# Optimization experiments

Hardware: AMD Instinct MI355X
Metric: run time of the kernel (lower is better)

## Reference

```python
import jax, jax.numpy as jnp
import numpy as np

WIN, DIL, PAD, H = 5, 1, 2, 8  # window, dilation, unfold padding, num_heads
C = 256
EPS = 1e-5

def _ln(z, g, b):
    m = jnp.mean(z, axis=-1, keepdims=True)
    v = jnp.mean((z - m) ** 2, axis=-1, keepdims=True)
    return (z - m) * jax.lax.rsqrt(v + EPS) * g + b

def setup_inputs() -> dict:
    key = jax.random.key(0)
    ks = jax.random.split(key, 16)
    s = 0.02
    d = {
        'x': jax.random.normal(ks[0], (32, C, 64, 25), jnp.float32),
        'ln1_g': jnp.ones((C,), jnp.float32), 'ln1_b': jnp.zeros((C,), jnp.float32),
        'q_w': jax.random.normal(ks[1], (C, C)) * s, 'q_b': jnp.zeros((C,)),
        'qa_w': jax.random.normal(ks[2], (C, H)) * s, 'qa_b': jnp.zeros((H,)),
        'k_w': jax.random.normal(ks[3], (C, C)) * s, 'k_b': jnp.zeros((C,)),
        'ka_w': jax.random.normal(ks[4], (C, H)) * s, 'ka_b': jnp.zeros((H,)),
        'v_w': jax.random.normal(ks[5], (C, C)) * s, 'v_b': jnp.zeros((C,)),
        't_w': jax.random.normal(ks[6], (C, C)) * s, 't_b': jnp.zeros((C,)),
        'p_w': jax.random.normal(ks[7], (C, C)) * s, 'p_b': jnp.zeros((C,)),
        'ffn_g': jnp.ones((C,)), 'ffn_b': jnp.zeros((C,)),
        'w1': jax.random.normal(ks[8], (C, C)) * s, 'b1': jnp.zeros((C,)),
        'w2': jax.random.normal(ks[9], (C, C)) * s, 'b2': jnp.zeros((C,)),
    }
    return d

def reference(x, ln1_g, ln1_b, q_w, q_b, qa_w, qa_b, k_w, k_b, ka_w, ka_b,
              v_w, v_b, t_w, t_b, p_w, p_b, ffn_g, ffn_b, w1, b1, w2, b2):
    N, Cc, T, V = x.shape
    hc = Cc // H
    scale = 1.0 / np.sqrt(hc)
    B, L = N * T, WIN * V
    xp = jnp.pad(x, ((0, 0), (0, 0), (PAD, PAD), (0, 0)))
    win = jnp.stack([xp[:, :, k * DIL:k * DIL + T, :] for k in range(WIN)], axis=2)  # (N,C,W,T,V)
    wx = win.transpose(0, 3, 2, 4, 1).reshape(B, L, Cc)
    nx = _ln(wx, ln1_g, ln1_b)
    # attention: softmax-pooled query
    q = nx @ q_w + q_b                                      # (B,L,C)
    qw = jax.nn.softmax(((q @ qa_w + qa_b) * scale).transpose(0, 2, 1), axis=-1)  # (B,H,L)
    qh = q.reshape(B, L, H, hc).transpose(0, 2, 1, 3)       # (B,H,L,hc)
    pq = jnp.einsum('bhl,bhld->bhd', qw, qh)                # (B,H,hc)
    k_ = nx @ k_w + k_b
    kq = k_ * pq.reshape(B, 1, Cc)
    kw = jax.nn.softmax(((kq @ ka_w + ka_b) * scale).transpose(0, 2, 1), axis=-1)
    kh = k_.reshape(B, L, H, hc).transpose(0, 2, 1, 3)
    pk = jnp.einsum('bhl,bhld->bhd', kw, kh)                # (B,H,hc)
    v_ = nx @ v_w + v_b
    vh = v_.reshape(B, L, H, hc).transpose(0, 2, 1, 3)
    kv = (vh * pk[:, :, None, :]).transpose(0, 2, 1, 3).reshape(B, L, Cc)
    kvh = (kv @ t_w + t_b).reshape(B, L, H, hc).transpose(0, 2, 1, 3)
    att = ((kvh + qh).transpose(0, 2, 1, 3).reshape(B, L, Cc)) @ p_w + p_b
    # average over window, residual with flattened x
    att = att.reshape(B, WIN, V, Cc).mean(axis=1)           # (B,V,C)
    att = att + x.transpose(0, 2, 3, 1).reshape(B, V, Cc)
    # FFN residual block
    f = _ln(att, ffn_g, ffn_b)
    f = jax.nn.gelu(f @ w1 + b1, approximate=False) @ w2 + b2
    y = f + att
    return y.reshape(N, T, V, Cc).transpose(0, 3, 1, 2)     # (N,C,T,V)
```

## Files before the change

### kernel.cpp

```cpp
#include <hip/hip_runtime.h>
#include <hip/hip_bf16.h>

typedef unsigned short u16b;
typedef __attribute__((ext_vector_type(8))) short short8;
typedef __attribute__((ext_vector_type(4))) float floatx4;

#define DEV static __device__ __forceinline__

DEV float sh2f(unsigned short s) { union { unsigned u; float f; } c; c.u = ((unsigned)s) << 16; return c.f; }
DEV unsigned short f2b(float f) {
    unsigned u = __float_as_uint(f);
    u += 0x7FFF + ((u >> 16) & 1);
    return (unsigned short)(u >> 16);
}

DEV void gload_lds16(const u16b* g, u16b* l) {
    __builtin_amdgcn_global_load_lds((const __attribute__((address_space(1))) void*)g,
                                     (__attribute__((address_space(3))) void*)l, 16, 0, 0);
}

constexpr int O_LN1G = 0, O_LN1B = 256, O_QB = 512, O_KB = 768, O_VB = 1024,
              O_TB = 1280, O_PB = 1536, O_FFNG = 1792, O_FFNB = 2048,
              O_B1 = 2304, O_B2 = 2560, O_QAB = 2816, O_KAB = 2824,
              O_QAW = 2832, O_KAW = 4880, O_CV = 6928;

__global__ void detect_k(const unsigned* __restrict__ xw, int* __restrict__ flag) {
    __shared__ int cnt;
    if (threadIdx.x == 0) cnt = 0;
    __syncthreads();
    int my = 0;
    for (int i = threadIdx.x; i < 4096; i += 256) {
        unsigned w = xw[i];
        unsigned e0 = (w >> 7) & 0xFFu;
        if (e0 >= 0xC0u) my++;
    }
    atomicAdd(&cnt, my);
    __syncthreads();
    if (threadIdx.x == 0) flag[0] = (cnt > 64) ? 1 : 0;
}

DEV unsigned short load_cvt(const void* src, size_t idx, int fp32) {
    return fp32 ? f2b(((const float*)src)[idx]) : ((const u16b*)src)[idx];
}

struct VecTab { const void* p[15]; int off[15]; int n[15]; };

__global__ __launch_bounds__(256)
void convert_vecs_k(VecTab tab, const int* __restrict__ flag, u16b* __restrict__ sv) {
    int e = blockIdx.x, fp32 = flag[0];
    const void* s = tab.p[e];
    int n = tab.n[e], off = tab.off[e];
    for (int i = threadIdx.x; i < n; i += 256)
        sv[off + i] = load_cvt(s, i, fp32);
}

struct W8 { const void* p[8]; unsigned dstoff[8]; unsigned rstride[8]; };

__global__ void wtrans_k(W8 tab, u16b* __restrict__ base, const int* __restrict__ flag) {
    __shared__ u16b tile[32][33];
    int fp32 = flag[0];
    const void* src = tab.p[blockIdx.z];
    u16b* dst = base + tab.dstoff[blockIdx.z];
    unsigned rs = tab.rstride[blockIdx.z];
    int c0 = blockIdx.x * 32, r0 = blockIdx.y * 32;
    int tx = threadIdx.x, ty = threadIdx.y;
#pragma unroll
    for (int i = 0; i < 32; i += 8)
        tile[ty + i][tx] = load_cvt(src, (size_t)(r0 + ty + i) * 256 + c0 + tx, fp32);
    __syncthreads();
#pragma unroll
    for (int i = 0; i < 32; i += 8)
        dst[(size_t)(c0 + ty + i) * rs + r0 + tx] = tile[tx][ty + i];
}

__global__ __launch_bounds__(256)
void transpose_in_k(const void* __restrict__ src, u16b* __restrict__ dst,
                    int rows, int cols, const int* __restrict__ flag) {
    __shared__ u16b tile[32][36];
    int fp32 = flag[0];
    int c0 = blockIdx.x * 32, r0 = blockIdx.y * 32;
    size_t zb = (size_t)blockIdx.z * rows * cols;
    int tid = threadIdx.x;
    int r = tid >> 3, c4 = (tid & 7) * 4;
    size_t sidx = zb + (size_t)(r0 + r) * cols + c0 + c4;
    if (fp32) {
        const float4 f4 = *(const float4*)((const float*)src + sidx);
        tile[r][c4]     = f2b(f4.x);
        tile[r][c4 + 1] = f2b(f4.y);
        tile[r][c4 + 2] = f2b(f4.z);
        tile[r][c4 + 3] = f2b(f4.w);
    } else {
        *(ushort4*)&tile[r][c4] = *(const ushort4*)((const u16b*)src + sidx);
    }
    __syncthreads();
    int c = tid >> 3, r4 = (tid & 7) * 4;
    ushort4 o;
    o.x = tile[r4][c]; o.y = tile[r4 + 1][c]; o.z = tile[r4 + 2][c]; o.w = tile[r4 + 3][c];
    *(ushort4*)&dst[zb + (size_t)(c0 + c) * rows + r0 + r4] = o;
}

__global__ __launch_bounds__(256)
void rowstats_k(const u16b* __restrict__ src, float2* __restrict__ st,
                int valid, int total) {
    int wv = threadIdx.x >> 6, lane = threadIdx.x & 63;
    int r = blockIdx.x * 4 + wv;
    if (r >= total) return;
    if (r >= valid) { if (lane == 0) st[r] = make_float2(0.f, 0.f); return; }
    int c = lane * 4;
    ushort4 raw = *(const ushort4*)&src[(size_t)r * 256 + c];
    float x0 = sh2f(raw.x), x1 = sh2f(raw.y), x2 = sh2f(raw.z), x3 = sh2f(raw.w);
    float s  = x0 + x1 + x2 + x3;
    float sq = x0 * x0 + x1 * x1 + x2 * x2 + x3 * x3;
#pragma unroll
    for (int o = 32; o; o >>= 1) { s += __shfl_xor(s, o); sq += __shfl_xor(sq, o); }
    float mean = s * (1.f / 256.f);
    float var  = sq * (1.f / 256.f) - mean * mean;
    if (lane == 0) st[r] = make_float2(mean, rsqrtf(var + 1e-5f));
}

__global__ __launch_bounds__(256)
void cvec_k(const u16b* __restrict__ pT, u16b* __restrict__ sv) {
    int j = threadIdx.x;
    float acc = sh2f(sv[O_PB + j]);
    const u16b* row = pT + (size_t)j * 256;
    for (int i = 0; i < 256; i += 8) {
        short8 t8 = *(const short8*)&sv[O_TB + i];
        short8 p8 = *(const short8*)&row[i];
#pragma unroll
        for (int u = 0; u < 8; ++u)
            acc += sh2f((unsigned short)t8[u]) * sh2f((unsigned short)p8[u]);
    }
    sv[O_CV + j] = f2b(acc);
}

template <int EPI, int LNA, int XY = 0, int STATS = 0>
__global__ __launch_bounds__(256, 4)
void gemm256(const u16b* __restrict__ A, int aStride, int K,
             const u16b* __restrict__ Wt,
             const u16b* __restrict__ bias, const u16b* __restrict__ addm,
             u16b* __restrict__ out, size_t osParam,
             const float2* __restrict__ stats, const float2* __restrict__ stats2,
             const u16b* __restrict__ gvec, const u16b* __restrict__ bvec,
             float2* __restrict__ statOut, const int* __restrict__ flag) {
    constexpr bool ALDS = (LNA == 0);
    __shared__ u16b As[64 * 72];
    __shared__ u16b Bs[8448];
    __shared__ float sg[256], sb[256];
    const int tid = threadIdx.x;
    const int m0 = (XY ? blockIdx.y : blockIdx.x) * 64;
    const int n0 = (XY ? blockIdx.x : blockIdx.y) * 128;
    const int wv = tid >> 6, lane = tid & 63;
    const int wrow = (wv >> 1) * 32, wcol = (wv & 1) * 64;
    const int fr = lane & 15;
    const int fq = lane >> 4;
    floatx4 acc[2][4];
    const floatx4 zero = {0.f, 0.f, 0.f, 0.f};
#pragma unroll
    for (int i = 0; i < 2; ++i)
#pragma unroll
        for (int j = 0; j < 4; ++j) acc[i][j] = zero;

    float2 strow[2];
    if (LNA) {
        sg[tid] = sh2f(gvec[tid]);
        sb[tid] = sh2f(bvec[tid]);
#pragma unroll
        for (int kk = 0; kk < 2; ++kk) {
            int r = m0 + (tid >> 3) + kk * 32;
            if (LNA == 2) {
                float2 a = stats[r], b = stats2[r];
                float mean = (a.x + b.x) * (1.f / 256.f);
                float var  = (a.y + b.y) * (1.f / 256.f) - mean * mean;
                strow[kk] = make_float2(mean, rsqrtf(var + 1e-5f));
            } else {
                strow[kk] = stats[r];
            }
        }
        __syncthreads();
    }

    for (int kt = 0; kt < K; kt += 64) {
        if (ALDS) {
#pragma unroll
            for (int kk = 0; kk < 2; ++kk) {
                int chunk = tid + kk * 256;
                int row = chunk >> 3, col = (chunk & 7) * 8;
                int scol = col ^ ((row & 7) << 3);
                gload_lds16(&A[(size_t)(m0 + row) * aStride + kt + scol], &As[chunk * 8]);
            }
        } else {
#pragma unroll
            for (int kk = 0; kk < 2; ++kk) {
                int chunk = tid + kk * 256;
                int row = chunk >> 3, col = (chunk & 7) * 8;
                union { uint4 u; unsigned short h[8]; } rw;
                rw.u = *(const uint4*)&A[(size_t)(m0 + row) * aStride + kt + col];
#pragma unroll
                for (int j = 0; j < 8; ++j) {
                    float f = sh2f(rw.h[j]);
                    f = (f - strow[kk].x) * strow[kk].y * sg[kt + col + j] + sb[kt + col + j];
                    rw.h[j] = f2b(f);
                }
                *(uint4*)&As[row * 72 + col] = rw.u;
            }
        }
#pragma unroll
        for (int kk = 0; kk < 4; ++kk) {
            int chunk = tid + kk * 256;
            int row = chunk >> 3, col = (chunk & 7) * 8;
            int scol = col ^ ((row & 7) << 3);
            gload_lds16(&Wt[(size_t)(n0 + row) * K + kt + scol], &Bs[chunk * 8]);
        }
        __syncthreads();
#pragma unroll
        for (int s = 0; s < 2; ++s) {
            short8 af[2], bfr[4];
#pragma unroll
            for (int i = 0; i < 2; ++i) {
                int ar = wrow + i * 16 + fr;
                if (ALDS)
                    af[i] = *(const short8*)((const char*)As +
                              ((ar * 128 + s * 64 + fq * 16) ^ ((ar & 7) << 4)));
                else
                    af[i] = *(short8*)&As[ar * 72 + s * 32 + fq * 8];
            }
#pragma unroll
            for (int j = 0; j < 4; ++j) {
                int br = wcol + j * 16 + fr;
                bfr[j] = *(const short8*)((const char*)Bs +
                          ((br * 128 + s * 64 + fq * 16) ^ ((br & 7) << 4)));
            }
#pragma unroll
            for (int i = 0; i < 2; ++i)
#pragma unroll
                for (int j = 0; j < 4; ++j)
                    acc[i][j] = __builtin_amdgcn_mfma_f32_16x16x32_bf16(af[i], bfr[j], acc[i][j], 0, 0, 0);
        }
        __syncthreads();
    }
    float bv[4];
#pragma unroll
    for (int j = 0; j < 4; ++j) bv[j] = bias ? sh2f(bias[n0 + wcol + j * 16 + fr]) : 0.f;

    if (EPI == 5) {
        u16b* CT = Bs;
#pragma unroll
        for (int kk = 0; kk < 4; ++kk) {
            int chunk = tid + kk * 256;
            int row = chunk >> 4, c8 = (chunk & 15) * 8;
            *(uint4*)&CT[row * 132 + c8] = *(const uint4*)&addm[(size_t)(m0 + row) * 256 + n0 + c8];
        }
        __syncthreads();
        int fp32o = flag[0];
#pragma unroll
        for (int i = 0; i < 2; ++i) {
            int lr0 = wrow + i * 16 + fq * 4;
            int row0 = m0 + lr0;
            int n = row0 / 1600;
            int tv = row0 - n * 1600;
#pragma unroll
            for (int j = 0; j < 4; ++j) {
                int lc = wcol + j * 16 + fr;
                int col = n0 + lc;
                float v4[4];
#pragma unroll
                for (int r = 0; r < 4; ++r)
                    v4[r] = acc[i][j][r] + bv[j] + sh2f(CT[(lr0 + r) * 132 + lc]);
                size_t oidx = ((size_t)n * 256 + col) * 1600 + tv;
                if (fp32o) {
                    float4 o = {v4[0], v4[1], v4[2], v4[3]};
                    *(float4*)((float*)out + oidx) = o;
                } else {
                    ushort4 o;
                    o.x = f2b(v4[0]); o.y = f2b(v4[1]); o.z = f2b(v4[2]); o.w = f2b(v4[3]);
                    *(ushort4*)&out[oidx] = o;
                }
            }
        }
    } else if (EPI == 2) {
        float* CTf = (float*)Bs;
#pragma unroll
        for (int half = 0; half < 2; ++half) {
            if ((wrow >> 5) == half) {
#pragma unroll
                for (int i = 0; i < 2; ++i)
#pragma unroll
                    for (int r = 0; r < 4; ++r) {
                        int lrow = i * 16 + fq * 4 + r;
#pragma unroll
                        for (int j = 0; j < 4; ++j)
                            CTf[lrow * 132 + wcol + j * 16 + fr] = acc[i][j][r] + bv[j];
                    }
            }
            __syncthreads();
#pragma unroll
            for (int kk = 0; kk < 2; ++kk) {
                int chunk = tid + kk * 256;
                int row = chunk >> 4, c8 = (chunk & 15) * 8;
                int grow = m0 + half * 32 + row, gcol = n0 + c8;
                union { uint4 u; unsigned short h[8]; } am, ow;
                am.u = *(const uint4*)&addm[(size_t)grow * 256 + gcol];
                float s1 = 0.f, s2 = 0.f;
#pragma unroll
                for (int u8 = 0; u8 < 8; ++u8) {
                    float v = CTf[row * 132 + c8 + u8] + sh2f(am.h[u8]);
                    s1 += v; s2 += v * v;
                    ow.h[u8] = f2b(v);
                }
                if (STATS) {
#pragma unroll
                    for (int mm = 1; mm < 16; mm <<= 1) {
                        s1 += __shfl_xor(s1, mm);
                        s2 += __shfl_xor(s2, mm);
                    }
                    if ((tid & 15) == 0)
                        statOut[(size_t)(n0 >> 7) * 51200 + grow] = make_float2(s1, s2);
                }
                *(uint4*)&out[(size_t)grow * 256 + gcol] = ow.u;
            }
            __syncthreads();
        }
    } else {
        u16b* CT = Bs;
#pragma unroll
        for (int i = 0; i < 2; ++i)
#pragma unroll
            for (int r = 0; r < 4; ++r) {
                int lrow = wrow + i * 16 + fq * 4 + r;
#pragma unroll
                for (int j = 0; j < 4; ++j) {
                    float val = acc[i][j][r] + bv[j];
                    if (EPI == 3) val = 0.5f * val * (1.0f + erff(val * 0.70710678118654752f));
                    CT[lrow * 132 + wcol + j * 16 + fr] = f2b(val);
                }
            }
        __syncthreads();
#pragma unroll
        for (int kk = 0; kk < 4; ++kk) {
            int chunk = tid + kk * 256;
            int row = chunk >> 4, c8 = (chunk & 15) * 8;
            int grow = m0 + row, gcol = n0 + c8;
            uint4 cw = *(const uint4*)&CT[row * 132 + c8];
            if (EPI == 4)      *(uint4*)&out[(size_t)(gcol >> 8) * osParam + (size_t)grow * 256 + (gcol & 255)] = cw;
            else               *(uint4*)&out[(size_t)grow * osParam + gcol] = cw;
        }
    }
}


DEV void logits_union(const u16b* __restrict__ S, const u16b* su, const int* srow,
                      float* slog, const u16b* __restrict__ sv, int aboff, int tid) {
    int wv = tid >> 6, lane = tid & 63;
    int fr = lane & 15, fq = lane >> 4;
    float abv = sh2f(sv[aboff + (fr & 7)]);
    for (int f = wv; f < 10; f += 8) {
        floatx4 acc = {0.f, 0.f, 0.f, 0.f};
        const u16b* Ar = S + (size_t)srow[f * 16 + fr] * 256;
#pragma unroll
        for (int s = 0; s < 8; ++s) {
            short8 a  = *(const short8*)&Ar[s * 32 + fq * 8];
            short8 bb = *(const short8*)&su[fr * 260 + s * 32 + fq * 8];
            acc = __builtin_amdgcn_mfma_f32_16x16x32_bf16(a, bb, acc, 0, 0, 0);
        }
#pragma unroll
        for (int r = 0; r < 4; ++r)
            slog[(f * 16 + fq * 4 + r) * 19 + fr] = (acc[r] + abv) * 0.17677669529663687f;
    }
}

template <int KC>
DEV void softmax16(const float* slog, float* wqA, float* wqB, int tid) {
    int wv = tid >> 6, lane = tid & 63;
#pragma unroll
    for (int c = 0; c < 2; ++c) {
        int combo = wv + c * 8;
        int dt = combo >> 3, h = combo & 7;
        int col = KC ? combo : h;
        const float* src = slog + (size_t)(dt * 25) * 19 + col;
        float v0 = (lane < 125) ? src[lane * 19] : -1e30f;
        float v1 = (lane + 64 < 125) ? src[(lane + 64) * 19] : -1e30f;
        float mx = fmaxf(v0, v1);
#pragma unroll
        for (int o = 32; o; o >>= 1) mx = fmaxf(mx, __shfl_xor(mx, o));
        float e0 = (lane < 125) ? __expf(v0 - mx) : 0.f;
        float e1 = (lane + 64 < 125) ? __expf(v1 - mx) : 0.f;
        float s = e0 + e1;
#pragma unroll
        for (int o = 32; o; o >>= 1) s += __shfl_xor(s, o);
        float inv = 1.f / s;
        float* dst = dt ? wqB : wqA;
        int off = dt ? 25 : 0;
        if (lane < 125) dst[(lane + off) * 9 + h] = e0 * inv;
        if (lane + 64 < 125) dst[(lane + 64 + off) * 9 + h] = e1 * inv;
    }
}

DEV void pool_union(const u16b* __restrict__ S, const int* srow,
                    const float* wqA, const float* wqB, float* scratch,
                    float* out0, float* out1, int tid) {
    int c8 = (tid & 31) * 8, h = c8 >> 5, ls = tid >> 5;
    float a0[8] = {0.f,0.f,0.f,0.f,0.f,0.f,0.f,0.f};
    float a1[8] = {0.f,0.f,0.f,0.f,0.f,0.f,0.f,0.f};
    for (int u = ls; u < 150; u += 16) {
        float w0 = wqA[u * 9 + h];
        float w1 = wqB[u * 9 + h];
        short8 d8 = *(const short8*)&S[(size_t)srow[u] * 256 + c8];
#pragma unroll
        for (int j = 0; j < 8; ++j) {
            float f = sh2f((unsigned short)d8[j]);
            a0[j] += w0 * f;
            a1[j] += w1 * f;
        }
    }
#pragma unroll
    for (int j = 0; j < 8; ++j) {
        a0[j] += __shfl_xor(a0[j], 32);
        a1[j] += __shfl_xor(a1[j], 32);
    }
    int wv = tid >> 6, lane = tid & 63;
    if (lane < 32) {
        float4 lo = {a0[0], a0[1], a0[2], a0[3]}, hi = {a0[4], a0[5], a0[6], a0[7]};
        *(float4*)&scratch[wv * 264 + c8]     = lo;
        *(float4*)&scratch[wv * 264 + c8 + 4] = hi;
    }
    __syncthreads();
    if (tid < 256) {
        float s = 0.f;
#pragma unroll
        for (int q = 0; q < 8; ++q) s += scratch[q * 264 + tid];
        out0[tid] = s;
    }
    __syncthreads();
    if (lane < 32) {
        float4 lo = {a1[0], a1[1], a1[2], a1[3]}, hi = {a1[4], a1[5], a1[6], a1[7]};
        *(float4*)&scratch[wv * 264 + c8]     = lo;
        *(float4*)&scratch[wv * 264 + c8 + 4] = hi;
    }
    __syncthreads();
    if (tid < 256) {
        float s = 0.f;
#pragma unroll
        for (int q = 0; q < 8; ++q) s += scratch[q * 264 + tid];
        out1[tid] = s;
    }
    __syncthreads();
}

DEV void wmean2(const u16b* __restrict__ S, const int* srow,
                const float* scale0, const float* scale1,
                u16b* __restrict__ CB, int base, int nb, int tid) {
    for (int i = tid; i < 800; i += 512) {
        int v = i >> 5, c8 = (i & 31) * 8;
        float s0[8] = {0.f,0.f,0.f,0.f,0.f,0.f,0.f,0.f};
        float s1[8] = {0.f,0.f,0.f,0.f,0.f,0.f,0.f,0.f};
#pragma unroll
        for (int w = 0; w < 6; ++w) {
            short8 d8 = *(const short8*)&S[(size_t)srow[w * 25 + v] * 256 + c8];
#pragma unroll
            for (int j = 0; j < 8; ++j) {
                float f = sh2f((unsigned short)d8[j]);
                if (w < 5)  s0[j] += f;
                if (w >= 1) s1[j] += f;
            }
        }
        unsigned short o0[8], o1[8];
#pragma unroll
        for (int j = 0; j < 8; ++j) {
            float m0 = s0[j] * 0.2f, m1 = s1[j] * 0.2f;
            if (scale0) { m0 *= scale0[c8 + j]; m1 *= scale1[c8 + j]; }
            o0[j] = f2b(m0); o1[j] = f2b(m1);
        }
        *(uint4*)&CB[((size_t)nb * 25 + v) * 512 + base + c8]       = *(uint4*)o0;
        *(uint4*)&CB[((size_t)(nb + 1) * 25 + v) * 512 + base + c8] = *(uint4*)o1;
    }
}

__global__ __launch_bounds__(512)
void pool_fused2(const u16b* __restrict__ qf, const u16b* __restrict__ kf,
                 const u16b* __restrict__ vf, const u16b* __restrict__ sv,
                 u16b* __restrict__ CB) {
    __shared__ int srow[160];
    __shared__ u16b su[16 * 260];
    __shared__ float slog[160 * 19];
    __shared__ float wqA[160 * 9], wqB[160 * 9];
    __shared__ float spq[2][256], spk[2][256];
    int bid = blockIdx.x;
    int b2 = ((bid & 7) << 7) | (bid >> 3);
    int n = b2 >> 5, t0 = (b2 & 31) * 2;
    int nb = n * 64 + t0;
    int tid = threadIdx.x;
    if (tid < 160) {
        int u = tid < 150 ? tid : 149;
        int tl = u / 25, v = u - tl * 25, tt = t0 + tl - 2;
        srow[tid] = ((unsigned)tt < 64u) ? (n * 64 + tt) * 25 + v : 51200;
    }
    for (int i = tid; i < 2048; i += 512) {
        int c = i >> 3, h = i & 7;
        su[h * 260 + c] = sv[O_QAW + i];
    }
    for (int i = tid; i < 1440; i += 512) { wqA[i] = 0.f; wqB[i] = 0.f; }
    __syncthreads();

    logits_union(qf, su, srow, slog, sv, O_QAB, tid);
    __syncthreads();
    softmax16<0>(slog, wqA, wqB, tid);
    __syncthreads();

    pool_union(qf, srow, wqA, wqB, slog, spq[0], spq[1], tid);

    wmean2(qf, srow, nullptr, nullptr, CB, 256, nb, tid);

    for (int i = tid; i < 4096; i += 512) {
        int c = i >> 4, h16 = i & 15;
        float w = sh2f(sv[O_KAW + c * 8 + (h16 & 7)]) * spq[h16 >> 3][c];
        su[h16 * 260 + c] = f2b(w);
    }
    for (int i = tid; i < 1440; i += 512) { wqA[i] = 0.f; wqB[i] = 0.f; }
    __syncthreads();

    logits_union(kf, su, srow, slog, sv, O_KAB, tid);
    __syncthreads();
    softmax16<1>(slog, wqA, wqB, tid);
    __syncthreads();

    pool_union(kf, srow, wqA, wqB, slog, spk[0], spk[1], tid);

    wmean2(vf, srow, spk[0], spk[1], CB, 0, nb, tid);
}

extern "C" void kernel_launch(void* const* d_in, const int* in_sizes, int n_in,
                              void* d_out, int out_size, void* d_ws, size_t ws_size,
                              hipStream_t stream) {
    (void)in_sizes; (void)n_in; (void)out_size; (void)ws_size;
    const void* x    = d_in[0];
    const void* ln1g = d_in[1];  const void* ln1b = d_in[2];
    const void* q_w  = d_in[3];  const void* q_b  = d_in[4];
    const void* qa_w = d_in[5];  const void* qa_b = d_in[6];
    const void* k_w  = d_in[7];  const void* k_b  = d_in[8];
    const void* ka_w = d_in[9];  const void* ka_b = d_in[10];
    const void* v_w  = d_in[11]; const void* v_b  = d_in[12];
    const void* t_w  = d_in[13]; const void* t_b  = d_in[14];
    const void* p_w  = d_in[15]; const void* p_b  = d_in[16];
    const void* ffng = d_in[17]; const void* ffnb = d_in[18];
    const void* w1   = d_in[19]; const void* b1   = d_in[20];
    const void* w2   = d_in[21]; const void* b2   = d_in[22];

    char* ws = (char*)d_ws;
    size_t off = 0;
    auto alloc = [&](size_t bytes) { void* p = ws + off; off += (bytes + 255) & ~(size_t)255; return p; };
    const size_t RPAD = 51328;
    int*    flag = (int*)alloc(256);
    u16b*   sv   = (u16b*)alloc(8192 * 2);
    u16b*   wT   = (u16b*)alloc((size_t)7 * 65536 * 2);
    u16b*   cW   = (u16b*)alloc((size_t)256 * 512 * 2);
    u16b*   xT   = (u16b*)alloc(RPAD * 256 * 2);
    u16b*   Bq   = (u16b*)alloc(RPAD * 256 * 2);
    u16b*   Bk   = (u16b*)alloc(RPAD * 256 * 2);
    u16b*   Bv   = (u16b*)alloc(RPAD * 256 * 2);
    u16b*   CB   = (u16b*)alloc((size_t)51200 * 512 * 2);
    u16b*   att  = (u16b*)alloc((size_t)51200 * 256 * 2);
    float2* st1  = (float2*)alloc(RPAD * 8);
    float2* st2p = (float2*)alloc((size_t)2 * 51200 * 8);

    u16b* pT  = wT + 3 * 65536;
    u16b* tT  = wT + 4 * 65536;
    u16b* w1T = wT + 5 * 65536;
    u16b* w2T = wT + 6 * 65536;

    detect_k<<<1, 256, 0, stream>>>((const unsigned*)x, flag);
    VecTab tab;
    const void* vp[15] = {ln1g, ln1b, q_b, k_b, v_b, t_b, p_b, ffng, ffnb, b1, b2, qa_b, ka_b, qa_w, ka_w};
    const int vo[15] = {O_LN1G, O_LN1B, O_QB, O_KB, O_VB, O_TB, O_PB, O_FFNG, O_FFNB, O_B1, O_B2, O_QAB, O_KAB, O_QAW, O_KAW};
    const int vn[15] = {256, 256, 256, 256, 256, 256, 256, 256, 256, 256, 256, 8, 8, 2048, 2048};
    for (int i = 0; i < 15; ++i) { tab.p[i] = vp[i]; tab.off[i] = vo[i]; tab.n[i] = vn[i]; }
    convert_vecs_k<<<15, 256, 0, stream>>>(tab, flag, sv);

    dim3 tb(32, 8);
    W8 wt;
    const void* wsrc[8] = {q_w, k_w, v_w, p_w, t_w, w1, w2, p_w};
    for (int i = 0; i < 8; ++i) {
        wt.p[i] = wsrc[i];
        wt.dstoff[i] = (i < 7) ? (unsigned)(i * 65536) : (unsigned)((cW + 256) - wT);
        wt.rstride[i] = (i < 7) ? 256u : 512u;
    }
    wtrans_k<<<dim3(8, 8, 8), tb, 0, stream>>>(wt, wT, flag);
    cvec_k<<<1, 256, 0, stream>>>(pT, sv);
    gemm256<0, 0><<<dim3(4, 2), 256, 0, stream>>>(pT, 256, 256, tT, nullptr, nullptr,
                                                  cW, 512, nullptr, nullptr, nullptr, nullptr,
                                                  nullptr, nullptr);
    transpose_in_k<<<dim3(50, 8, 32), 256, 0, stream>>>(x, xT, 256, 1600, flag);
    rowstats_k<<<12832, 256, 0, stream>>>(xT, st1, 51200, 51328);
    gemm256<4, 1, 1><<<dim3(6, 802), 256, 0, stream>>>(xT, 256, 256, wT, sv + O_QB, nullptr,
                                                       Bq, RPAD * 256, st1, nullptr,
                                                       sv + O_LN1G, sv + O_LN1B, nullptr, nullptr);
    pool_fused2<<<1024, 512, 0, stream>>>(Bq, Bk, Bv, sv, CB);
    gemm256<2, 0, 1, 1><<<dim3(2, 800), 256, 0, stream>>>(CB, 512, 512, cW, sv + O_CV, xT,
                                                          att, 256, nullptr, nullptr,
                                                          nullptr, nullptr, st2p, nullptr);
    gemm256<3, 2, 1><<<dim3(2, 800), 256, 0, stream>>>(att, 256, 256, w1T, sv + O_B1, nullptr,
                                                       Bq, 256, st2p, st2p + 51200,
                                                       sv + O_FFNG, sv + O_FFNB, nullptr, nullptr);
    gemm256<5, 0, 1><<<dim3(2, 800), 256, 0, stream>>>(Bq, 256, 256, w2T, sv + O_B2, att,
                                                       (u16b*)d_out, 0, nullptr, nullptr,
                                                       nullptr, nullptr, nullptr, flag);
}
```

Measured before the change: 369.6 us.

## Fuse query-attention logits into QKV GEMM epilogue and merge pool reductions

The QKV projection GEMM now computes the per-row query-attention logits (q @ qa_w) in its epilogue for the q column blocks, writing two partial halves to a new float buffer. The pooling kernel then reads those precomputed logits instead of re-reading q rows and running an MFMA logits pass. The two pooled reductions in pool_union are also split into a sweep and a reduce that share one barrier, which removes several __syncthreads, and one redundant zeroing loop is dropped. The cost is extra epilogue work, a 2048-entry weight load into shared memory, and shuffle reductions inside the GEMM. The logits are also computed from bf16-rounded q values.

```diff
diff --git a/kernel.cpp b/kernel.cpp
--- a/kernel.cpp
+++ b/kernel.cpp
@@ -23,6 +23,7 @@
               O_TB = 1280, O_PB = 1536, O_FFNG = 1792, O_FFNB = 2048,
               O_B1 = 2304, O_B2 = 2560, O_QAB = 2816, O_KAB = 2824,
               O_QAW = 2832, O_KAW = 4880, O_CV = 6928;
+constexpr int RPADC = 51328;
 
 __global__ void detect_k(const unsigned* __restrict__ xw, int* __restrict__ flag) {
     __shared__ int cnt;
@@ -133,7 +134,7 @@
     sv[O_CV + j] = f2b(acc);
 }
 
-template <int EPI, int LNA, int XY = 0, int STATS = 0>
+template <int EPI, int LNA, int XY = 0, int STATS = 0, int LQ = 0>
 __global__ __launch_bounds__(256, 4)
 void gemm256(const u16b* __restrict__ A, int aStride, int K,
              const u16b* __restrict__ Wt,
@@ -141,7 +142,8 @@
              u16b* __restrict__ out, size_t osParam,
              const float2* __restrict__ stats, const float2* __restrict__ stats2,
              const u16b* __restrict__ gvec, const u16b* __restrict__ bvec,
-             float2* __restrict__ statOut, const int* __restrict__ flag) {
+             float2* __restrict__ statOut, const int* __restrict__ flag,
+             const u16b* __restrict__ qawp, float* __restrict__ lqOut) {
     constexpr bool ALDS = (LNA == 0);
     __shared__ u16b As[64 * 72];
     __shared__ u16b Bs[8448];
@@ -322,6 +324,11 @@
         }
     } else {
         u16b* CT = Bs;
+        float* qawf = (float*)As;
+        const bool doLQ = LQ && (n0 < 256);
+        if (doLQ) {
+            for (int i = tid; i < 2048; i += 256) qawf[i] = sh2f(qawp[i]);
+        }
 #pragma unroll
         for (int i = 0; i < 2; ++i)
 #pragma unroll
@@ -343,6 +350,28 @@
             uint4 cw = *(const uint4*)&CT[row * 132 + c8];
             if (EPI == 4)      *(uint4*)&out[(size_t)(gcol >> 8) * osParam + (size_t)grow * 256 + (gcol & 255)] = cw;
             else               *(uint4*)&out[(size_t)grow * osParam + gcol] = cw;
+            if (doLQ) {
+                union { uint4 u; unsigned short h[8]; } cc; cc.u = cw;
+                float s[8] = {0.f, 0.f, 0.f, 0.f, 0.f, 0.f, 0.f, 0.f};
+#pragma unroll
+                for (int j = 0; j < 8; ++j) {
+                    float v = sh2f(cc.h[j]);
+                    const float* qr = qawf + (size_t)(gcol + j) * 8;
+#pragma unroll
+                    for (int h = 0; h < 8; ++h) s[h] += v * qr[h];
+                }
+#pragma unroll
+                for (int mm = 1; mm < 16; mm <<= 1)
+#pragma unroll
+                    for (int h = 0; h < 8; ++h) s[h] += __shfl_xor(s[h], mm);
+                if ((tid & 15) == 0) {
+                    float* dst = lqOut + ((size_t)(n0 >> 7) * RPADC + grow) * 8;
+                    float4 lo = {s[0], s[1], s[2], s[3]};
+                    float4 hi = {s[4], s[5], s[6], s[7]};
+                    *(float4*)dst = lo;
+                    *(float4*)(dst + 4) = hi;
+                }
+            }
         }
     }
 }
@@ -395,9 +424,9 @@
     }
 }
 
-DEV void pool_union(const u16b* __restrict__ S, const int* srow,
-                    const float* wqA, const float* wqB, float* scratch,
-                    float* out0, float* out1, int tid) {
+DEV void pool_sweep2(const u16b* __restrict__ S, const int* srow,
+                     const float* wqA, const float* wqB,
+                     float* scrA, float* scrB, int tid) {
     int c8 = (tid & 31) * 8, h = c8 >> 5, ls = tid >> 5;
     float a0[8] = {0.f,0.f,0.f,0.f,0.f,0.f,0.f,0.f};
     float a1[8] = {0.f,0.f,0.f,0.f,0.f,0.f,0.f,0.f};
@@ -419,31 +448,29 @@
     }
     int wv = tid >> 6, lane = tid & 63;
     if (lane < 32) {
-        float4 lo = {a0[0], a0[1], a0[2], a0[3]}, hi = {a0[4], a0[5], a0[6], a0[7]};
-        *(float4*)&scratch[wv * 264 + c8]     = lo;
-        *(float4*)&scratch[wv * 264 + c8 + 4] = hi;
-    }
-    __syncthreads();
+        float4 lo0 = {a0[0], a0[1], a0[2], a0[3]}, hi0 = {a0[4], a0[5], a0[6], a0[7]};
+        *(float4*)&scrA[wv * 264 + c8]     = lo0;
+        *(float4*)&scrA[wv * 264 + c8 + 4] = hi0;
+        float4 lo1 = {a1[0], a1[1], a1[2], a1[3]}, hi1 = {a1[4], a1[5], a1[6], a1[7]};
+        *(float4*)&scrB[wv * 260 + c8]     = lo1;
+        *(float4*)&scrB[wv * 260 + c8 + 4] = hi1;
+    }
+}
+
+DEV void pool_reduce2(const float* scrA, const float* scrB,
+                      float* out0, float* out1, int tid) {
     if (tid < 256) {
         float s = 0.f;
 #pragma unroll
-        for (int q = 0; q < 8; ++q) s += scratch[q * 264 + tid];
+        for (int q = 0; q < 8; ++q) s += scrA[q * 264 + tid];
         out0[tid] = s;
-    }
-    __syncthreads();
-    if (lane < 32) {
-        float4 lo = {a1[0], a1[1], a1[2], a1[3]}, hi = {a1[4], a1[5], a1[6], a1[7]};
-        *(float4*)&scratch[wv * 264 + c8]     = lo;
-        *(float4*)&scratch[wv * 264 + c8 + 4] = hi;
-    }
-    __syncthreads();
-    if (tid < 256) {
+    } else {
+        int t2 = tid - 256;
         float s = 0.f;
 #pragma unroll
-        for (int q = 0; q < 8; ++q) s += scratch[q * 264 + tid];
-        out1[tid] = s;
-    }
-    __syncthreads();
+        for (int q = 0; q < 8; ++q) s += scrB[q * 260 + t2];
+        out1[t2] = s;
+    }
 }
 
 DEV void wmean2(const u16b* __restrict__ S, const int* srow,
@@ -477,10 +504,10 @@
 
 __global__ __launch_bounds__(512)
 void pool_fused2(const u16b* __restrict__ qf, const u16b* __restrict__ kf,
-                 const u16b* __restrict__ vf, const u16b* __restrict__ sv,
-                 u16b* __restrict__ CB) {
+                 const u16b* __restrict__ vf, const float* __restrict__ Lqp,
+                 const u16b* __restrict__ sv, u16b* __restrict__ CB) {
     __shared__ int srow[160];
-    __shared__ u16b su[16 * 260];
+    __shared__ alignas(16) u16b su[16 * 260];
     __shared__ float slog[160 * 19];
     __shared__ float wqA[160 * 9], wqB[160 * 9];
     __shared__ float spq[2][256], spk[2][256];
@@ -494,28 +521,30 @@
         int tl = u / 25, v = u - tl * 25, tt = t0 + tl - 2;
         srow[tid] = ((unsigned)tt < 64u) ? (n * 64 + tt) * 25 + v : 51200;
     }
-    for (int i = tid; i < 2048; i += 512) {
-        int c = i >> 3, h = i & 7;
-        su[h * 260 + c] = sv[O_QAW + i];
-    }
     for (int i = tid; i < 1440; i += 512) { wqA[i] = 0.f; wqB[i] = 0.f; }
     __syncthreads();
 
-    logits_union(qf, su, srow, slog, sv, O_QAB, tid);
+    for (int i = tid; i < 1200; i += 512) {
+        int u = i >> 3, h = i & 7;
+        size_t row = (size_t)srow[u];
+        float lq = Lqp[row * 8 + h] + Lqp[(size_t)RPADC * 8 + row * 8 + h] + sh2f(sv[O_QAB + h]);
+        slog[u * 19 + h] = lq * 0.17677669529663687f;
+    }
     __syncthreads();
     softmax16<0>(slog, wqA, wqB, tid);
     __syncthreads();
 
-    pool_union(qf, srow, wqA, wqB, slog, spq[0], spq[1], tid);
-
+    pool_sweep2(qf, srow, wqA, wqB, slog, (float*)su, tid);
     wmean2(qf, srow, nullptr, nullptr, CB, 256, nb, tid);
+    __syncthreads();
+    pool_reduce2(slog, (float*)su, spq[0], spq[1], tid);
+    __syncthreads();
 
     for (int i = tid; i < 4096; i += 512) {
         int c = i >> 4, h16 = i & 15;
         float w = sh2f(sv[O_KAW + c * 8 + (h16 & 7)]) * spq[h16 >> 3][c];
         su[h16 * 260 + c] = f2b(w);
     }
-    for (int i = tid; i < 1440; i += 512) { wqA[i] = 0.f; wqB[i] = 0.f; }
     __syncthreads();
 
     logits_union(kf, su, srow, slog, sv, O_KAB, tid);
@@ -523,7 +552,10 @@
     softmax16<1>(slog, wqA, wqB, tid);
     __syncthreads();
 
-    pool_union(kf, srow, wqA, wqB, slog, spk[0], spk[1], tid);
+    pool_sweep2(kf, srow, wqA, wqB, slog, (float*)su, tid);
+    __syncthreads();
+    pool_reduce2(slog, (float*)su, spk[0], spk[1], tid);
+    __syncthreads();
 
     wmean2(vf, srow, spk[0], spk[1], CB, 0, nb, tid);
 }
@@ -548,7 +580,7 @@
     char* ws = (char*)d_ws;
     size_t off = 0;
     auto alloc = [&](size_t bytes) { void* p = ws + off; off += (bytes + 255) & ~(size_t)255; return p; };
-    const size_t RPAD = 51328;
+    const size_t RPAD = RPADC;
     int*    flag = (int*)alloc(256);
     u16b*   sv   = (u16b*)alloc(8192 * 2);
     u16b*   wT   = (u16b*)alloc((size_t)7 * 65536 * 2);
@@ -561,6 +593,7 @@
     u16b*   att  = (u16b*)alloc((size_t)51200 * 256 * 2);
     float2* st1  = (float2*)alloc(RPAD * 8);
     float2* st2p = (float2*)alloc((size_t)2 * 51200 * 8);
+    float*  Lqp  = (float*)alloc((size_t)2 * RPAD * 8 * 4);
 
     u16b* pT  = wT + 3 * 65536;
     u16b* tT  = wT + 4 * 65536;
@@ -587,20 +620,24 @@
     cvec_k<<<1, 256, 0, stream>>>(pT, sv);
     gemm256<0, 0><<<dim3(4, 2), 256, 0, stream>>>(pT, 256, 256, tT, nullptr, nullptr,
                                                   cW, 512, nullptr, nullptr, nullptr, nullptr,
-                                                  nullptr, nullptr);
+                                                  nullptr, nullptr, nullptr, nullptr);
     transpose_in_k<<<dim3(50, 8, 32), 256, 0, stream>>>(x, xT, 256, 1600, flag);
     rowstats_k<<<12832, 256, 0, stream>>>(xT, st1, 51200, 51328);
-    gemm256<4, 1, 1><<<dim3(6, 802), 256, 0, stream>>>(xT, 256, 256, wT, sv + O_QB, nullptr,
-                                                       Bq, RPAD * 256, st1, nullptr,
-                                                       sv + O_LN1G, sv + O_LN1B, nullptr, nullptr);
-    pool_fused2<<<1024, 512, 0, stream>>>(Bq, Bk, Bv, sv, CB);
+    gemm256<4, 1, 1, 0, 1><<<dim3(6, 802), 256, 0, stream>>>(xT, 256, 256, wT, sv + O_QB, nullptr,
+                                                             Bq, RPAD * 256, st1, nullptr,
+                                                             sv + O_LN1G, sv + O_LN1B, nullptr, nullptr,
+                                                             sv + O_QAW, Lqp);
+    pool_fused2<<<1024, 512, 0, stream>>>(Bq, Bk, Bv, Lqp, sv, CB);
     gemm256<2, 0, 1, 1><<<dim3(2, 800), 256, 0, stream>>>(CB, 512, 512, cW, sv + O_CV, xT,
                                                           att, 256, nullptr, nullptr,
-                                                          nullptr, nullptr, st2p, nullptr);
+                                                          nullptr, nullptr, st2p, nullptr,
+                                                          nullptr, nullptr);
     gemm256<3, 2, 1><<<dim3(2, 800), 256, 0, stream>>>(att, 256, 256, w1T, sv + O_B1, nullptr,
                                                        Bq, 256, st2p, st2p + 51200,
-                                                       sv + O_FFNG, sv + O_FFNB, nullptr, nullptr);
+                                                       sv + O_FFNG, sv + O_FFNB, nullptr, nullptr,
+                                                       nullptr, nullptr);
     gemm256<5, 0, 1><<<dim3(2, 800), 256, 0, stream>>>(Bq, 256, 256, w2T, sv + O_B2, att,
                                                        (u16b*)d_out, 0, nullptr, nullptr,
-                                                       nullptr, nullptr, nullptr, flag);
-}
+                                                       nullptr, nullptr, nullptr, flag,
+                                                       nullptr, nullptr);
+}
```

Measured after the change: 426.9 us. +15.5%, slower.

## Fuse LN1 row statistics into QKV GEMM and split pooling reductions

Applied to the files above, without the earlier changes.

Drops the separate rowstats kernel. Each QKV GEMM block now reads its 64 rows of xT in full and computes mean and rstd itself, with an 8-lane shuffle reduction. This removes a kernel launch and a round trip of the stats through global memory, but the stats are recomputed redundantly by each of the 6 column blocks. In the pooling kernel, the two weighted-pool reductions now write to separate scratch buffers so they can be reduced together, which cuts several syncthreads and overlaps the first reduction with wmean2. A redundant zeroing loop is also removed.

```diff
diff --git a/kernel.cpp b/kernel.cpp
--- a/kernel.cpp
+++ b/kernel.cpp
@@ -23,6 +23,7 @@
               O_TB = 1280, O_PB = 1536, O_FFNG = 1792, O_FFNB = 2048,
               O_B1 = 2304, O_B2 = 2560, O_QAB = 2816, O_KAB = 2824,
               O_QAW = 2832, O_KAW = 4880, O_CV = 6928;
+constexpr int VALIDC = 51200;
 
 __global__ void detect_k(const unsigned* __restrict__ xw, int* __restrict__ flag) {
     __shared__ int cnt;
@@ -97,25 +98,6 @@
     ushort4 o;
     o.x = tile[r4][c]; o.y = tile[r4 + 1][c]; o.z = tile[r4 + 2][c]; o.w = tile[r4 + 3][c];
     *(ushort4*)&dst[zb + (size_t)(c0 + c) * rows + r0 + r4] = o;
-}
-
-__global__ __launch_bounds__(256)
-void rowstats_k(const u16b* __restrict__ src, float2* __restrict__ st,
-                int valid, int total) {
-    int wv = threadIdx.x >> 6, lane = threadIdx.x & 63;
-    int r = blockIdx.x * 4 + wv;
-    if (r >= total) return;
-    if (r >= valid) { if (lane == 0) st[r] = make_float2(0.f, 0.f); return; }
-    int c = lane * 4;
-    ushort4 raw = *(const ushort4*)&src[(size_t)r * 256 + c];
-    float x0 = sh2f(raw.x), x1 = sh2f(raw.y), x2 = sh2f(raw.z), x3 = sh2f(raw.w);
-    float s  = x0 + x1 + x2 + x3;
-    float sq = x0 * x0 + x1 * x1 + x2 * x2 + x3 * x3;
-#pragma unroll
-    for (int o = 32; o; o >>= 1) { s += __shfl_xor(s, o); sq += __shfl_xor(sq, o); }
-    float mean = s * (1.f / 256.f);
-    float var  = sq * (1.f / 256.f) - mean * mean;
-    if (lane == 0) st[r] = make_float2(mean, rsqrtf(var + 1e-5f));
 }
 
 __global__ __launch_bounds__(256)
@@ -164,16 +146,40 @@
     if (LNA) {
         sg[tid] = sh2f(gvec[tid]);
         sb[tid] = sh2f(bvec[tid]);
-#pragma unroll
-        for (int kk = 0; kk < 2; ++kk) {
-            int r = m0 + (tid >> 3) + kk * 32;
-            if (LNA == 2) {
+        if (LNA == 1) {
+#pragma unroll
+            for (int kk = 0; kk < 2; ++kk) {
+                int chunk = tid + kk * 256;
+                int row = chunk >> 3, col = (chunk & 7) * 8;
+                float s1 = 0.f, s2 = 0.f;
+#pragma unroll
+                for (int kt2 = 0; kt2 < 256; kt2 += 64) {
+                    union { uint4 u; unsigned short h[8]; } rw;
+                    rw.u = *(const uint4*)&A[(size_t)(m0 + row) * aStride + kt2 + col];
+#pragma unroll
+                    for (int j = 0; j < 8; ++j) {
+                        float f = sh2f(rw.h[j]);
+                        s1 += f; s2 += f * f;
+                    }
+                }
+#pragma unroll
+                for (int mm = 1; mm < 8; mm <<= 1) {
+                    s1 += __shfl_xor(s1, mm);
+                    s2 += __shfl_xor(s2, mm);
+                }
+                float mean = s1 * (1.f / 256.f);
+                float var  = s2 * (1.f / 256.f) - mean * mean;
+                strow[kk] = (m0 + row < VALIDC) ? make_float2(mean, rsqrtf(var + 1e-5f))
+                                                : make_float2(0.f, 0.f);
+            }
+        } else {
+#pragma unroll
+            for (int kk = 0; kk < 2; ++kk) {
+                int r = m0 + (tid >> 3) + kk * 32;
                 float2 a = stats[r], b = stats2[r];
                 float mean = (a.x + b.x) * (1.f / 256.f);
                 float var  = (a.y + b.y) * (1.f / 256.f) - mean * mean;
                 strow[kk] = make_float2(mean, rsqrtf(var + 1e-5f));
-            } else {
-                strow[kk] = stats[r];
             }
         }
         __syncthreads();
@@ -395,9 +401,9 @@
     }
 }
 
-DEV void pool_union(const u16b* __restrict__ S, const int* srow,
-                    const float* wqA, const float* wqB, float* scratch,
-                    float* out0, float* out1, int tid) {
+DEV void pool_sweep2(const u16b* __restrict__ S, const int* srow,
+                     const float* wqA, const float* wqB,
+                     float* scrA, float* scrB, int tid) {
     int c8 = (tid & 31) * 8, h = c8 >> 5, ls = tid >> 5;
     float a0[8] = {0.f,0.f,0.f,0.f,0.f,0.f,0.f,0.f};
     float a1[8] = {0.f,0.f,0.f,0.f,0.f,0.f,0.f,0.f};
@@ -419,31 +425,29 @@
     }
     int wv = tid >> 6, lane = tid & 63;
     if (lane < 32) {
-        float4 lo = {a0[0], a0[1], a0[2], a0[3]}, hi = {a0[4], a0[5], a0[6], a0[7]};
-        *(float4*)&scratch[wv * 264 + c8]     = lo;
-        *(float4*)&scratch[wv * 264 + c8 + 4] = hi;
-    }
-    __syncthreads();
+        float4 lo0 = {a0[0], a0[1], a0[2], a0[3]}, hi0 = {a0[4], a0[5], a0[6], a0[7]};
+        *(float4*)&scrA[wv * 264 + c8]     = lo0;
+        *(float4*)&scrA[wv * 264 + c8 + 4] = hi0;
+        float4 lo1 = {a1[0], a1[1], a1[2], a1[3]}, hi1 = {a1[4], a1[5], a1[6], a1[7]};
+        *(float4*)&scrB[wv * 260 + c8]     = lo1;
+        *(float4*)&scrB[wv * 260 + c8 + 4] = hi1;
+    }
+}
+
+DEV void pool_reduce2(const float* scrA, const float* scrB,
+                      float* out0, float* out1, int tid) {
     if (tid < 256) {
         float s = 0.f;
 #pragma unroll
-        for (int q = 0; q < 8; ++q) s += scratch[q * 264 + tid];
+        for (int q = 0; q < 8; ++q) s += scrA[q * 264 + tid];
         out0[tid] = s;
-    }
-    __syncthreads();
-    if (lane < 32) {
-        float4 lo = {a1[0], a1[1], a1[2], a1[3]}, hi = {a1[4], a1[5], a1[6], a1[7]};
-        *(float4*)&scratch[wv * 264 + c8]     = lo;
-        *(float4*)&scratch[wv * 264 + c8 + 4] = hi;
-    }
-    __syncthreads();
-    if (tid < 256) {
+    } else {
+        int t2 = tid - 256;
         float s = 0.f;
 #pragma unroll
-        for (int q = 0; q < 8; ++q) s += scratch[q * 264 + tid];
-        out1[tid] = s;
-    }
-    __syncthreads();
+        for (int q = 0; q < 8; ++q) s += scrB[q * 260 + t2];
+        out1[t2] = s;
+    }
 }
 
 DEV void wmean2(const u16b* __restrict__ S, const int* srow,
@@ -480,7 +484,7 @@
                  const u16b* __restrict__ vf, const u16b* __restrict__ sv,
                  u16b* __restrict__ CB) {
     __shared__ int srow[160];
-    __shared__ u16b su[16 * 260];
+    __shared__ alignas(16) u16b su[16 * 260];
     __shared__ float slog[160 * 19];
     __shared__ float wqA[160 * 9], wqB[160 * 9];
     __shared__ float spq[2][256], spk[2][256];
@@ -506,16 +510,17 @@
     softmax16<0>(slog, wqA, wqB, tid);
     __syncthreads();
 
-    pool_union(qf, srow, wqA, wqB, slog, spq[0], spq[1], tid);
-
+    pool_sweep2(qf, srow, wqA, wqB, slog, (float*)su, tid);
     wmean2(qf, srow, nullptr, nullptr, CB, 256, nb, tid);
+    __syncthreads();
+    pool_reduce2(slog, (float*)su, spq[0], spq[1], tid);
+    __syncthreads();
 
     for (int i = tid; i < 4096; i += 512) {
         int c = i >> 4, h16 = i & 15;
         float w = sh2f(sv[O_KAW + c * 8 + (h16 & 7)]) * spq[h16 >> 3][c];
         su[h16 * 260 + c] = f2b(w);
     }
-    for (int i = tid; i < 1440; i += 512) { wqA[i] = 0.f; wqB[i] = 0.f; }
     __syncthreads();
 
     logits_union(kf, su, srow, slog, sv, O_KAB, tid);
@@ -523,7 +528,10 @@
     softmax16<1>(slog, wqA, wqB, tid);
     __syncthreads();
 
-    pool_union(kf, srow, wqA, wqB, slog, spk[0], spk[1], tid);
+    pool_sweep2(kf, srow, wqA, wqB, slog, (float*)su, tid);
+    __syncthreads();
+    pool_reduce2(slog, (float*)su, spk[0], spk[1], tid);
+    __syncthreads();
 
     wmean2(vf, srow, spk[0], spk[1], CB, 0, nb, tid);
 }
@@ -559,7 +567,6 @@
     u16b*   Bv   = (u16b*)alloc(RPAD * 256 * 2);
     u16b*   CB   = (u16b*)alloc((size_t)51200 * 512 * 2);
     u16b*   att  = (u16b*)alloc((size_t)51200 * 256 * 2);
-    float2* st1  = (float2*)alloc(RPAD * 8);
     float2* st2p = (float2*)alloc((size_t)2 * 51200 * 8);
 
     u16b* pT  = wT + 3 * 65536;
@@ -589,9 +596,8 @@
                                                   cW, 512, nullptr, nullptr, nullptr, nullptr,
                                                   nullptr, nullptr);
     transpose_in_k<<<dim3(50, 8, 32), 256, 0, stream>>>(x, xT, 256, 1600, flag);
-    rowstats_k<<<12832, 256, 0, stream>>>(xT, st1, 51200, 51328);
     gemm256<4, 1, 1><<<dim3(6, 802), 256, 0, stream>>>(xT, 256, 256, wT, sv + O_QB, nullptr,
-                                                       Bq, RPAD * 256, st1, nullptr,
+                                                       Bq, RPAD * 256, nullptr, nullptr,
                                                        sv + O_LN1G, sv + O_LN1B, nullptr, nullptr);
     pool_fused2<<<1024, 512, 0, stream>>>(Bq, Bk, Bv, sv, CB);
     gemm256<2, 0, 1, 1><<<dim3(2, 800), 256, 0, stream>>>(CB, 512, 512, cW, sv + O_CV, xT,
```

After: 370.8 us (median of 2 runs). Within noise of the previous version (+0.3%).
